# Kernel tuning notes

Measured on AMD Instinct MI355X. Metric: run time of the kernel, lower is better.

Reference implementation:

```python
import jax, jax.numpy as jnp
import numpy as np

N, E, D, L, G = 50000, 800000, 96, 4, 256
FI, PI, EI = 128, 16, 16


def setup_inputs() -> dict:
    key = jax.random.key(0)
    ks = jax.random.split(key, 40)
    w = lambda k, s: (jax.random.normal(k, s, jnp.float32) * 0.02)
    inp = {
        'h': jax.random.normal(ks[0], (N, FI), jnp.float32),
        'e': jax.random.normal(ks[1], (E, EI), jnp.float32),
        'p': jax.random.normal(ks[2], (N, PI), jnp.float32),
        'edge_index': jax.random.randint(ks[3], (2, E), 0, N),
        'batch': jnp.sort(jax.random.randint(ks[4], (N,), 0, G)),
        # embedding linears
        'h_emb_w': w(ks[5], (FI, D)), 'h_emb_b': jnp.zeros((D,), jnp.float32),
        'e_emb_w': w(ks[6], (EI, D)), 'e_emb_b': jnp.zeros((D,), jnp.float32),
        'p_emb_w': w(ks[7], (PI, D)), 'p_emb_b': jnp.zeros((D,), jnp.float32),
        # per-layer weights, stacked over L layers
        'gate_w': w(ks[8], (L, 3 * D, D)), 'gate_b': jnp.zeros((L, D), jnp.float32),
        'hps_w': w(ks[9], (L, 2 * D, D)), 'hps_b': jnp.zeros((L, D), jnp.float32),
        'hpr_w': w(ks[10], (L, 2 * D, D)), 'hpr_b': jnp.zeros((L, D), jnp.float32),
        'ps_w': w(ks[11], (L, D, D)), 'ps_b': jnp.zeros((L, D), jnp.float32),
        'pr_w': w(ks[12], (L, D, D)), 'pr_b': jnp.zeros((L, D), jnp.float32),
        # readout MLP
        'ro1_w': w(ks[13], (2 * D, D)), 'ro1_b': jnp.zeros((D,), jnp.float32),
        'ro2_w': w(ks[14], (D, 1)), 'ro2_b': jnp.zeros((1,), jnp.float32),
    }
    return inp


def reference(h, e, p, edge_index, batch,
              h_emb_w, h_emb_b, e_emb_w, e_emb_b, p_emb_w, p_emb_b,
              gate_w, gate_b, hps_w, hps_b, hpr_w, hpr_b,
              ps_w, ps_b, pr_w, pr_b, ro1_w, ro1_b, ro2_w, ro2_b):
    send, rec = edge_index[0], edge_index[1]
    n_nodes = h.shape[0]
    h = h @ h_emb_w + h_emb_b
    e = e @ e_emb_w + e_emb_b
    p = p @ p_emb_w + p_emb_b
    n_layers = gate_w.shape[0]
    for l in range(n_layers):
        # gather h at send/rec, gate over concat [E, 3D]
        eta_hat = jax.nn.sigmoid(
            jnp.concatenate([h[send], h[rec], e], axis=1) @ gate_w[l] + gate_b[l])
        eta = eta_hat / jnp.sum(eta_hat, axis=1, keepdims=True)
        hp = jnp.concatenate([h, p], axis=1)  # [N, 2D]
        h_msg = eta * (hp[send] @ hps_w[l] + hps_b[l])
        h_agg = jax.ops.segment_sum(h_msg, rec, num_segments=n_nodes)
        h_new = hp @ hpr_w[l] + hpr_b[l] + h_agg
        p_msg = eta * (p[send] @ ps_w[l] + ps_b[l])
        p_agg = jax.ops.segment_sum(p_msg, rec, num_segments=n_nodes)
        p_new = h_new @ pr_w[l] + pr_b[l] + p_agg  # uses updated h (matches torch layer)
        h = h + jax.nn.relu(h_new)
        e = e + jax.nn.relu(eta_hat)
        p = p + jnp.tanh(p_new)
    h_pool = jax.ops.segment_sum(h, batch, num_segments=G)  # global_add_pool
    p_pool = jax.ops.segment_sum(p, batch, num_segments=G)
    x = jnp.concatenate([h_pool, p_pool], axis=1) @ ro1_w + ro1_b
    x = jax.nn.relu(x) @ ro2_w + ro2_b
    return x.squeeze(-1)  # [G]
```

## Files before the change

### kernel.cpp

```cpp
#include <hip/hip_runtime.h>

typedef unsigned short u16;
typedef unsigned int u32;

#define NN 50000
#define EE 800000
#define DD 96
#define LL 4
#define GG 256
#define NPW 8
#define NPB (4*NPW)

typedef __bf16 bf16x8 __attribute__((ext_vector_type(8)));
typedef float f32x4 __attribute__((ext_vector_type(4)));

__device__ __forceinline__ u16 f2bf(float x){
  u32 u = __float_as_uint(x);
  u32 r = (u + 0x7FFFu + ((u >> 16) & 1u)) >> 16;
  return (u16)r;
}
__device__ __forceinline__ float bf2f(u16 b){
  return __uint_as_float(((u32)b) << 16);
}
__device__ __forceinline__ float bfx(const uint4& q, int i){
  u32 w = (i < 2) ? q.x : (i < 4) ? q.y : (i < 6) ? q.z : q.w;
  u32 h = (i & 1) ? (w >> 16) : (w & 0xFFFFu);
  return __uint_as_float(h << 16);
}
union BQ { uint4 q; bf16x8 v; };
__device__ __forceinline__ bf16x8 asbf(uint4 q){ BQ u; u.q = q; return u.v; }
__device__ __forceinline__ f32x4 mfma16(uint4 a, uint4 b, f32x4 c){
  return __builtin_amdgcn_mfma_f32_16x16x32_bf16(asbf(a), asbf(b), c, 0, 0, 0);
}
__device__ __forceinline__ uint4 pack8(const float* v){
  uint4 q;
  q.x = (u32)f2bf(v[0]) | ((u32)f2bf(v[1]) << 16);
  q.y = (u32)f2bf(v[2]) | ((u32)f2bf(v[3]) << 16);
  q.z = (u32)f2bf(v[4]) | ((u32)f2bf(v[5]) << 16);
  q.w = (u32)f2bf(v[6]) | ((u32)f2bf(v[7]) << 16);
  return q;
}
__device__ __forceinline__ uint4 packrow(const float* hsrc, const float* psrc, int row, int kbase){
  const float* src = (kbase < 96) ? (hsrc + (size_t)row*96 + kbase)
                                  : (psrc + (size_t)row*96 + (kbase - 96));
  float4 a0 = ((const float4*)src)[0];
  float4 a1 = ((const float4*)src)[1];
  float v[8] = {a0.x,a0.y,a0.z,a0.w,a1.x,a1.y,a1.z,a1.w};
  return pack8(v);
}

__global__ void k_diag(float* out, float val){
  int i = blockIdx.x*64 + threadIdx.x;
  if (i < GG) out[i] = val;
}

__global__ void k_zero(int* counts){
  int i = blockIdx.x*256 + threadIdx.x;
  if (i < NN) counts[i] = 0;
}
__global__ void k_hist(const int* rec, int* counts){
  int e = blockIdx.x*256 + threadIdx.x;
  if (e < EE) atomicAdd(&counts[rec[e]], 1);
}
__global__ void k_scan(const int* counts, int* cursor, int* node_start){
  __shared__ int wsum[16];
  __shared__ int carry_s;
  const int tid = threadIdx.x, lane = tid & 63, wid = tid >> 6;
  if (tid == 0) carry_s = 0;
  __syncthreads();
  for (int base = 0; base < NN; base += 1024){
    int i = base + tid;
    int v = (i < NN) ? counts[i] : 0;
    int x = v;
    #pragma unroll
    for (int d = 1; d < 64; d <<= 1){
      int t = __shfl_up(x, d);
      if (lane >= d) x += t;
    }
    if (lane == 63) wsum[wid] = x;
    __syncthreads();
    if (wid == 0 && lane < 16){
      int y = wsum[lane];
      #pragma unroll
      for (int d = 1; d < 16; d <<= 1){ int t = __shfl_up(y, d); if (lane >= d) y += t; }
      wsum[lane] = y;
    }
    __syncthreads();
    int woff = (wid == 0) ? 0 : wsum[wid-1];
    if (i < NN){
      int ex = carry_s + woff + x - v;
      cursor[i] = ex;
      node_start[i] = ex;
    }
    __syncthreads();
    if (tid == 1023) carry_s += wsum[15];
    __syncthreads();
  }
  if (tid == 0) node_start[NN] = EE;
}
__global__ void k_scatter(const int* send, const int* rec, int* cursor,
                          int* ss, int* rs, int* perm){
  int e = blockIdx.x*256 + threadIdx.x;
  if (e >= EE) return;
  int r = rec[e];
  int pos = atomicAdd(&cursor[r], 1);
  ss[pos] = send[e];
  rs[pos] = r;
  perm[pos] = e;
}

__global__ void k_prep(const float* gate_w, const float* gate_b,
    const float* hps_w, const float* hps_b,
    const float* hpr_w, const float* hpr_b,
    const float* ps_w, const float* ps_b,
    const float* pr_w,
    const float* h_emb_w, const float* p_emb_w, const float* e_emb_w,
    u16* Wt_cat, float* bias_cat, u16* Wt_e, u16* Wt_pr, u16* Wt_emb, u16* Wt_ee){
  int i = blockIdx.x*256 + threadIdx.x;
  const int S0 = LL*480*192, S1 = LL*96*96, S2 = LL*96*96, S3 = 192*160, S4 = 96*32, S5 = LL*480;
  if (i < S0){
    int l = i / (480*192); int r = i % (480*192);
    int j = r / 192, k = r % 192;
    int g = j / 96, jj = j % 96;
    float v = 0.f;
    if (g == 0){ if (k < 96) v = gate_w[((size_t)l*288 + k)*96 + jj]; }
    else if (g == 1){ if (k < 96) v = gate_w[((size_t)l*288 + 96 + k)*96 + jj]; }
    else if (g == 2){ if (k >= 96) v = ps_w[((size_t)l*96 + (k-96))*96 + jj]; }
    else if (g == 3){ v = hps_w[((size_t)l*192 + k)*96 + jj]; }
    else            { v = hpr_w[((size_t)l*192 + k)*96 + jj]; }
    Wt_cat[i] = f2bf(v);
    return;
  }
  i -= S0;
  if (i < S1){
    int l = i / 9216, r = i % 9216; int j = r / 96, k = r % 96;
    Wt_e[i] = f2bf(gate_w[((size_t)l*288 + 192 + k)*96 + j]);
    return;
  }
  i -= S1;
  if (i < S2){
    int l = i / 9216, r = i % 9216; int j = r / 96, k = r % 96;
    Wt_pr[i] = f2bf(pr_w[((size_t)l*96 + k)*96 + j]);
    return;
  }
  i -= S2;
  if (i < S3){
    int j = i / 160, k = i % 160;
    float v = 0.f;
    if (j < 96){ if (k < 128) v = h_emb_w[k*96 + j]; }
    else { if (k >= 128 && k < 144) v = p_emb_w[(k-128)*96 + (j-96)]; }
    Wt_emb[i] = f2bf(v);
    return;
  }
  i -= S3;
  if (i < S4){
    int j = i / 32, k = i % 32;
    Wt_ee[i] = f2bf(k < 16 ? e_emb_w[k*96 + j] : 0.f);
    return;
  }
  i -= S4;
  if (i < S5){
    int l = i / 480, j = i % 480;
    int g = j / 96, jj = j % 96;
    float v = 0.f;
    if (g == 1) v = gate_b[l*96 + jj];
    else if (g == 2) v = ps_b[l*96 + jj];
    else if (g == 3) v = hps_b[l*96 + jj];
    else if (g == 4) v = hpr_b[l*96 + jj];
    bias_cat[i] = v;
  }
}

__global__ __launch_bounds__(256,2) void k_emb_hp(const float* h_in, const float* p_in,
    const u16* Wt_emb, const float* h_emb_b, const float* p_emb_b,
    float* h, float* p){
  __shared__ u16 lds[96*168];
  const int tid = threadIdx.x;
  const int j0 = blockIdx.y * 96;
  for (int c = tid; c < 96*160/8; c += 256){
    int jr = c / 20, kc = c % 20;
    *(uint4*)&lds[jr*168 + kc*8] = *(const uint4*)(Wt_emb + (size_t)(j0+jr)*160 + kc*8);
  }
  __syncthreads();
  const int wave = tid >> 6, lane = tid & 63;
  const int quad = lane >> 4, l15 = lane & 15;
  const int base = blockIdx.x*256 + wave*64;
  f32x4 zero = {0.f,0.f,0.f,0.f};
  f32x4 acc[4][6];
  #pragma unroll
  for (int rg=0; rg<4; ++rg){
    #pragma unroll
    for (int ct=0; ct<6; ++ct) acc[rg][ct] = zero;
  }
  for (int ks = 0; ks < 5; ++ks){
    uint4 aq[4];
    #pragma unroll
    for (int rg = 0; rg < 4; ++rg){
      int row = base + rg*16 + l15;
      int chunk = ks*4 + quad;
      float v[8] = {0.f,0.f,0.f,0.f,0.f,0.f,0.f,0.f};
      if (row < NN){
        if (chunk < 16){
          const float4* sp = (const float4*)(h_in + (size_t)row*128 + chunk*8);
          float4 a0 = sp[0], a1 = sp[1];
          v[0]=a0.x; v[1]=a0.y; v[2]=a0.z; v[3]=a0.w; v[4]=a1.x; v[5]=a1.y; v[6]=a1.z; v[7]=a1.w;
        } else if (chunk < 18){
          const float4* sp = (const float4*)(p_in + (size_t)row*16 + (chunk-16)*8);
          float4 a0 = sp[0], a1 = sp[1];
          v[0]=a0.x; v[1]=a0.y; v[2]=a0.z; v[3]=a0.w; v[4]=a1.x; v[5]=a1.y; v[6]=a1.z; v[7]=a1.w;
        }
      }
      aq[rg] = pack8(v);
    }
    #pragma unroll
    for (int ct = 0; ct < 6; ++ct){
      uint4 bq = *(const uint4*)&lds[(ct*16+l15)*168 + ks*32 + quad*8];
      #pragma unroll
      for (int rg = 0; rg < 4; ++rg) acc[rg][ct] = mfma16(aq[rg], bq, acc[rg][ct]);
    }
  }
  #pragma unroll
  for (int rg=0; rg<4; ++rg){
    #pragma unroll
    for (int ct=0; ct<6; ++ct){
      #pragma unroll
      for (int reg=0; reg<4; ++reg){
        int row = base + rg*16 + quad*4 + reg;
        if (row < NN){
          int col = j0 + ct*16 + l15;
          float v = acc[rg][ct][reg] + (col < 96 ? h_emb_b[col] : p_emb_b[col-96]);
          if (col < 96) h[(size_t)row*96 + col] = v;
          else          p[(size_t)row*96 + col - 96] = v;
        }
      }
    }
  }
}

__global__ __launch_bounds__(256,2) void k_emb_e(const float* e_in, const int* perm,
    const u16* Wt_ee, const float* e_emb_b, u16* e_bf){
  __shared__ u16 lds[96*40];
  const int tid = threadIdx.x;
  for (int c = tid; c < 96*32/8; c += 256){
    int jr = c >> 2, kc = c & 3;
    *(uint4*)&lds[jr*40 + kc*8] = *(const uint4*)(Wt_ee + jr*32 + kc*8);
  }
  __syncthreads();
  const int wave = tid >> 6, lane = tid & 63;
  const int quad = lane >> 4, l15 = lane & 15;
  const int base = blockIdx.x*256 + wave*64;
  f32x4 zero = {0.f,0.f,0.f,0.f};
  f32x4 acc[4][6];
  #pragma unroll
  for (int rg=0; rg<4; ++rg){
    #pragma unroll
    for (int ct=0; ct<6; ++ct) acc[rg][ct] = zero;
  }
  uint4 aq[4];
  #pragma unroll
  for (int rg = 0; rg < 4; ++rg){
    int row = base + rg*16 + l15;
    int src = perm[row];
    float v[8] = {0.f,0.f,0.f,0.f,0.f,0.f,0.f,0.f};
    if (quad < 2){
      const float4* sp = (const float4*)(e_in + (size_t)src*16 + quad*8);
      float4 a0 = sp[0], a1 = sp[1];
      v[0]=a0.x; v[1]=a0.y; v[2]=a0.z; v[3]=a0.w; v[4]=a1.x; v[5]=a1.y; v[6]=a1.z; v[7]=a1.w;
    }
    aq[rg] = pack8(v);
  }
  #pragma unroll
  for (int ct = 0; ct < 6; ++ct){
    uint4 bq = *(const uint4*)&lds[(ct*16+l15)*40 + quad*8];
    #pragma unroll
    for (int rg = 0; rg < 4; ++rg) acc[rg][ct] = mfma16(aq[rg], bq, acc[rg][ct]);
  }
  #pragma unroll
  for (int rg=0; rg<4; ++rg){
    #pragma unroll
    for (int ct=0; ct<6; ++ct){
      #pragma unroll
      for (int reg=0; reg<4; ++reg){
        int row = base + rg*16 + quad*4 + reg;
        int col = ct*16 + l15;
        e_bf[(size_t)row*96 + col] = f2bf(acc[rg][ct][reg] + e_emb_b[col]);
      }
    }
  }
}

__global__ __launch_bounds__(256,2) void k_pre(const float* h, const float* p,
    const u16* Wt_cat, const float* bias_cat, int l,
    u16* Gt, float* h_agg){
  __shared__ u16 lds[96*200];
  const int tid = threadIdx.x;
  const int group = blockIdx.y;
  const u16* W = Wt_cat + ((size_t)l*480 + group*96)*192;
  for (int c = tid; c < 96*192/8; c += 256){
    int jr = c / 24, kc = c % 24;
    *(uint4*)&lds[jr*200 + kc*8] = *(const uint4*)(W + jr*192 + kc*8);
  }
  __syncthreads();
  const int wave = tid >> 6, lane = tid & 63;
  const int quad = lane >> 4, l15 = lane & 15;
  const int base = blockIdx.x*64 + wave*16;
  f32x4 zero = {0.f,0.f,0.f,0.f};
  f32x4 acc[6];
  #pragma unroll
  for (int ct=0; ct<6; ++ct) acc[ct] = zero;
  const int ks0 = (group == 2) ? 3 : 0;
  const int ks1 = (group <= 1) ? 3 : 6;
  uint4 zeroq = {0u,0u,0u,0u};
  const int arow = base + l15;
  for (int ks = ks0; ks < ks1; ++ks){
    int kbase = ks*32 + quad*8;
    uint4 aq = (arow < NN) ? packrow(h, p, arow, kbase) : zeroq;
    #pragma unroll
    for (int ct = 0; ct < 6; ++ct){
      uint4 bq = *(const uint4*)&lds[(ct*16+l15)*200 + ks*32 + quad*8];
      acc[ct] = mfma16(aq, bq, acc[ct]);
    }
  }
  const float* bptr = bias_cat + l*480 + group*96;
  if (group == 4){
    #pragma unroll
    for (int ct=0; ct<6; ++ct){
      #pragma unroll
      for (int reg=0; reg<4; ++reg){
        int row = base + quad*4 + reg;
        if (row < NN){
          int col = ct*16 + l15;
          h_agg[(size_t)row*96 + col] = acc[ct][reg] + bptr[col];
        }
      }
    }
  } else {
    float bv[6];
    #pragma unroll
    for (int ct=0; ct<6; ++ct) bv[ct] = bptr[ct*16 + l15];
    #pragma unroll
    for (int reg=0; reg<4; ++reg){
      int row = base + quad*4 + reg;
      if (row < NN){
        float v[8];
        #pragma unroll
        for (int ct=0; ct<6; ++ct) v[ct] = acc[ct][reg] + bv[ct];
        v[6] = 0.f; v[7] = 0.f;
        *(uint4*)(Gt + (size_t)row*512 + group*128 + l15*8) = pack8(v);
      }
    }
  }
}

__global__ __launch_bounds__(256,3) void k_edge(u16* e_bf, const u16* Wt_e_l,
    const int* ss, const int* rs, const int* node_start,
    const u16* Gt, float* h_agg, float* p_agg){
  __shared__ u16 lds[96*104];
  __shared__ float accLDS[4][2][NPW*96];
  const int tid = threadIdx.x;
  for (int c = tid; c < 96*96/8; c += 256){
    int jr = c / 12, kc = c % 12;
    *(uint4*)&lds[jr*104 + kc*8] = *(const uint4*)(Wt_e_l + jr*96 + kc*8);
  }
  __syncthreads();
  const int wave = tid >> 6, lane = tid & 63;
  const int quad = lane >> 4, l15 = lane & 15;
  const int n0 = blockIdx.x*NPB + wave*NPW;
  if (n0 >= NN) return;
  const int n1 = min(n0 + NPW, NN);
  const int ws0 = node_start[n0], ws1 = node_start[n1];
  float* accH = accLDS[wave][0];
  float* accP = accLDS[wave][1];
  for (int k = lane; k < NPW*96; k += 64){ accH[k] = 0.f; accP[k] = 0.f; }

  for (int tb = ws0; tb < ws1; tb += 64){
    f32x4 zero = {0.f,0.f,0.f,0.f};
    f32x4 acc[4][6];
    #pragma unroll
    for (int rg=0; rg<4; ++rg){
      #pragma unroll
      for (int ct=0; ct<6; ++ct) acc[rg][ct] = zero;
    }
    #pragma unroll
    for (int ks = 0; ks < 3; ++ks){
      uint4 aq[4];
      #pragma unroll
      for (int rg = 0; rg < 4; ++rg){
        int row = tb + rg*16 + l15;
        if (row > EE-1) row = EE-1;
        aq[rg] = *(const uint4*)(e_bf + (size_t)row*96 + ks*32 + quad*8);
      }
      #pragma unroll
      for (int ct = 0; ct < 6; ++ct){
        uint4 bq = *(const uint4*)&lds[(ct*16+l15)*104 + ks*32 + quad*8];
        #pragma unroll
        for (int rg = 0; rg < 4; ++rg) acc[rg][ct] = mfma16(aq[rg], bq, acc[rg][ct]);
      }
    }
    #pragma unroll
    for (int rg=0; rg<4; ++rg){
      const int e0 = tb + rg*16 + quad*4;
      if (e0 >= ws1) continue;
      int4 s4 = *(const int4*)(ss + e0);
      int4 r4 = *(const int4*)(rs + e0);
      const int sArr[4] = {s4.x, s4.y, s4.z, s4.w};
      const int rArr[4] = {r4.x, r4.y, r4.z, r4.w};
      float hacc[6], pacc[6];
      #pragma unroll
      for (int ct=0; ct<6; ++ct){ hacc[ct]=0.f; pacc[ct]=0.f; }
      int curR = rArr[0];
      uint4 grq = *(const uint4*)(Gt + (size_t)curR*512 + 128 + l15*8);
      #pragma unroll
      for (int reg=0; reg<4; ++reg){
        const int edge = e0 + reg;
        if (edge < ws1){
          const int s = sArr[reg], r = rArr[reg];
          if (r != curR){
            int nb = (curR - n0)*96;
            #pragma unroll
            for (int ct=0; ct<6; ++ct){
              int col = ct*16 + l15;
              atomicAdd(&accH[nb+col], hacc[ct]);
              atomicAdd(&accP[nb+col], pacc[ct]);
              hacc[ct]=0.f; pacc[ct]=0.f;
            }
            curR = r;
            grq = *(const uint4*)(Gt + (size_t)curR*512 + 128 + l15*8);
          }
          const u16* Gs = Gt + (size_t)s*512 + l15*8;
          uint4 aqv = *(const uint4*)(Gs);
          uint4 sqv = *(const uint4*)(Gs + 256);
          uint4 mqv = *(const uint4*)(Gs + 384);
          float eh[6]; float rsum = 0.f;
          #pragma unroll
          for (int ct=0; ct<6; ++ct){
            float z = acc[rg][ct][reg] + bfx(aqv, ct) + bfx(grq, ct);
            float v = 1.f/(1.f + __expf(-z));
            eh[ct] = v; rsum += v;
          }
          rsum += __shfl_xor(rsum, 1); rsum += __shfl_xor(rsum, 2);
          rsum += __shfl_xor(rsum, 4); rsum += __shfl_xor(rsum, 8);
          float inv = 1.f / rsum;
          #pragma unroll
          for (int ct=0; ct<6; ++ct){
            int col = ct*16 + l15;
            size_t ei = (size_t)edge*96 + col;
            e_bf[ei] = f2bf(bf2f(e_bf[ei]) + eh[ct]);
            float eta = eh[ct] * inv;
            hacc[ct] += eta * bfx(mqv, ct);
            pacc[ct] += eta * bfx(sqv, ct);
          }
        }
      }
      {
        int nb = (curR - n0)*96;
        #pragma unroll
        for (int ct=0; ct<6; ++ct){
          int col = ct*16 + l15;
          atomicAdd(&accH[nb+col], hacc[ct]);
          atomicAdd(&accP[nb+col], pacc[ct]);
        }
      }
    }
  }
  const int nk = (n1 - n0)*96;
  for (int k = lane; k < nk; k += 64){
    size_t gi = (size_t)n0*96 + k;
    h_agg[gi] += accH[k];
    p_agg[gi]  = accP[k];
  }
}

__global__ __launch_bounds__(256,2) void k_pr(const float* h_agg, const u16* Wt_pr_l,
    const float* pr_b_l, const float* p_agg, float* p, float* h){
  __shared__ u16 lds[96*104];
  const int tid = threadIdx.x;
  for (int c = tid; c < 96*96/8; c += 256){
    int jr = c / 12, kc = c % 12;
    *(uint4*)&lds[jr*104 + kc*8] = *(const uint4*)(Wt_pr_l + jr*96 + kc*8);
  }
  __syncthreads();
  const int wave = tid >> 6, lane = tid & 63;
  const int quad = lane >> 4, l15 = lane & 15;
  const int base = blockIdx.x*64 + wave*16;
  f32x4 zero = {0.f,0.f,0.f,0.f};
  f32x4 acc[6];
  #pragma unroll
  for (int ct=0; ct<6; ++ct) acc[ct] = zero;
  uint4 zeroq = {0u,0u,0u,0u};
  const int arow = base + l15;
  #pragma unroll
  for (int ks = 0; ks < 3; ++ks){
    int kbase = ks*32 + quad*8;
    uint4 aq = (arow < NN) ? packrow(h_agg, h_agg, arow, kbase) : zeroq;
    #pragma unroll
    for (int ct = 0; ct < 6; ++ct){
      uint4 bq = *(const uint4*)&lds[(ct*16+l15)*104 + ks*32 + quad*8];
      acc[ct] = mfma16(aq, bq, acc[ct]);
    }
  }
  #pragma unroll
  for (int ct=0; ct<6; ++ct){
    #pragma unroll
    for (int reg=0; reg<4; ++reg){
      int row = base + quad*4 + reg;
      if (row < NN){
        int col = ct*16 + l15;
        size_t idx = (size_t)row*96 + col;
        float v = acc[ct][reg] + pr_b_l[col] + p_agg[idx];
        float vv = fminf(fmaxf(v, -15.f), 15.f);
        float ex = __expf(2.f*vv);
        float th = (ex - 1.f) / (ex + 1.f);
        p[idx] += th;
        h[idx] += fmaxf(h_agg[idx], 0.f);
      }
    }
  }
}

__global__ void k_off(const int* batch, int* starts){
  int g = threadIdx.x;
  int lo = 0, hi = NN;
  while (lo < hi){ int mid = (lo + hi) >> 1; if (batch[mid] < g) lo = mid + 1; else hi = mid; }
  starts[g] = lo;
  if (g == 0) starts[GG] = NN;
}

__global__ void k_pool(const float* h, const float* p, const int* starts, float* pool){
  int g = blockIdx.x, t = threadIdx.x;
  int a = starts[g], b = starts[g+1];
  const float* src = (t < 96) ? h : p;
  int c = (t < 96) ? t : (t - 96);
  float s = 0.f;
  for (int n = a; n < b; ++n) s += src[(size_t)n*96 + c];
  pool[g*192 + t] = s;
}

__global__ void k_ro(const float* pool, const float* ro1_w, const float* ro1_b,
                     const float* ro2_w, const float* ro2_b, float* out){
  __shared__ float red[96];
  int g = blockIdx.x, j = threadIdx.x;
  if (j < 96){
    float a = ro1_b[j];
    for (int k = 0; k < 192; ++k) a += pool[g*192 + k] * ro1_w[k*96 + j];
    red[j] = fmaxf(a, 0.f) * ro2_w[j];
  }
  __syncthreads();
  if (j == 0){
    float s = 0.f;
    for (int k = 0; k < 96; ++k) s += red[k];
    out[g] = s + ro2_b[0];
  }
}

extern "C" void kernel_launch(void* const* d_in, const int* in_sizes, int n_in,
                              void* d_out, int out_size, void* d_ws, size_t ws_size,
                              hipStream_t stream){
  const float* in_h    = (const float*)d_in[0];
  const float* in_e    = (const float*)d_in[1];
  const float* in_p    = (const float*)d_in[2];
  const int*   eidx    = (const int*)d_in[3];
  const int*   batch   = (const int*)d_in[4];
  const float* h_emb_w = (const float*)d_in[5];
  const float* h_emb_b = (const float*)d_in[6];
  const float* e_emb_w = (const float*)d_in[7];
  const float* e_emb_b = (const float*)d_in[8];
  const float* p_emb_w = (const float*)d_in[9];
  const float* p_emb_b = (const float*)d_in[10];
  const float* gate_w  = (const float*)d_in[11];
  const float* gate_b  = (const float*)d_in[12];
  const float* hps_w   = (const float*)d_in[13];
  const float* hps_b   = (const float*)d_in[14];
  const float* hpr_w   = (const float*)d_in[15];
  const float* hpr_b   = (const float*)d_in[16];
  const float* ps_w    = (const float*)d_in[17];
  const float* ps_b    = (const float*)d_in[18];
  const float* pr_w    = (const float*)d_in[19];
  const float* pr_b    = (const float*)d_in[20];
  const float* ro1_w   = (const float*)d_in[21];
  const float* ro1_b   = (const float*)d_in[22];
  const float* ro2_w   = (const float*)d_in[23];
  const float* ro2_b   = (const float*)d_in[24];
  float* out = (float*)d_out;
  (void)in_sizes; (void)n_in; (void)out_size;

  u16* Gt = (u16*)d_in[1];

  char* w = (char*)d_ws;
  size_t off = 0;
  auto alloc = [&](size_t bytes)->char*{
    char* pt = w + off;
    off = (off + bytes + 255) & ~(size_t)255;
    return pt;
  };
  u16*   e_bf     = (u16*)alloc((size_t)EE*96*2);
  float* h        = (float*)alloc((size_t)NN*96*4);
  float* p        = (float*)alloc((size_t)NN*96*4);
  float* h_agg    = (float*)alloc((size_t)NN*96*4);
  float* p_agg    = (float*)alloc((size_t)NN*96*4);
  u16*   Wt_cat   = (u16*)alloc((size_t)LL*480*192*2);
  u16*   Wt_e     = (u16*)alloc((size_t)LL*96*96*2);
  u16*   Wt_pr    = (u16*)alloc((size_t)LL*96*96*2);
  float* bias_cat = (float*)alloc((size_t)LL*480*4);
  int*   perm     = (int*)alloc((size_t)EE*4);
  int*   ss       = (int*)alloc((size_t)EE*4);
  int*   rs       = (int*)alloc((size_t)EE*4);
  int*   counts   = (int*)alloc((size_t)NN*4);
  int*   cursor   = (int*)alloc((size_t)NN*4);
  int*   node_start = (int*)alloc((size_t)(NN+1)*4);
  char*  scratch  = alloc(197888);
  u16*   Wt_emb   = (u16*)scratch;
  u16*   Wt_ee    = (u16*)(scratch + 61440);
  float* pool     = (float*)scratch;
  int*   starts   = (int*)(scratch + 196608);
  const size_t NEED = off;

  if (ws_size < NEED){
    k_diag<<<4, 64, 0, stream>>>(out, (float)(ws_size >> 20));
    return;
  }

  const int* send = eidx;
  const int* rec  = eidx + EE;

  k_zero<<<196, 256, 0, stream>>>(counts);
  k_hist<<<3125, 256, 0, stream>>>(rec, counts);
  k_scan<<<1, 1024, 0, stream>>>(counts, cursor, node_start);
  k_scatter<<<3125, 256, 0, stream>>>(send, rec, cursor, ss, rs, perm);

  k_prep<<<1868, 256, 0, stream>>>(gate_w, gate_b, hps_w, hps_b, hpr_w, hpr_b,
      ps_w, ps_b, pr_w, h_emb_w, p_emb_w, e_emb_w,
      Wt_cat, bias_cat, Wt_e, Wt_pr, Wt_emb, Wt_ee);
  k_emb_hp<<<dim3(196,2), 256, 0, stream>>>(in_h, in_p, Wt_emb, h_emb_b, p_emb_b, h, p);
  k_emb_e<<<3125, 256, 0, stream>>>(in_e, perm, Wt_ee, e_emb_b, e_bf);

  const int edge_blocks = (NN + NPB - 1) / NPB;
  const int row_blocks  = (NN + 63) / 64;
  for (int l = 0; l < LL; ++l){
    k_pre<<<dim3(row_blocks,5), 256, 0, stream>>>(h, p, Wt_cat, bias_cat, l, Gt, h_agg);
    k_edge<<<edge_blocks, 256, 0, stream>>>(e_bf, Wt_e + (size_t)l*96*96, ss, rs,
                                            node_start, Gt, h_agg, p_agg);
    k_pr<<<row_blocks, 256, 0, stream>>>(h_agg, Wt_pr + (size_t)l*96*96, pr_b + l*96,
                                         p_agg, p, h);
  }

  k_off<<<1, 256, 0, stream>>>(batch, starts);
  k_pool<<<GG, 192, 0, stream>>>(h, p, starts, pool);
  k_ro<<<GG, 128, 0, stream>>>(pool, ro1_w, ro1_b, ro2_w, ro2_b, out);
}
```

Before: 2.174 ms.

## Stage edge-state updates through LDS and skip last-layer edge writeback

The edge kernel now loads each edge tile's bf16 features into registers once and keeps them. Previously each edge did a scalar 2-byte read-modify-write of e per column. Instead the sigmoid outputs are staged in a per-wave LDS buffer, added to the register-held tile, and written back as coalesced 16-byte stores. The final layer skips the edge update entirely because e is never read afterwards. The cost is more registers and LDS, so occupancy drops from 3 to 2 blocks per SIMD.

```diff
diff --git a/kernel.cpp b/kernel.cpp
--- a/kernel.cpp
+++ b/kernel.cpp
@@ -26,6 +26,16 @@
   u32 w = (i < 2) ? q.x : (i < 4) ? q.y : (i < 6) ? q.z : q.w;
   u32 h = (i & 1) ? (w >> 16) : (w & 0xFFFFu);
   return __uint_as_float(h << 16);
+}
+__device__ __forceinline__ u32 bfadd2(u32 a, u32 b){
+  float a0 = __uint_as_float(a << 16), a1 = __uint_as_float(a & 0xFFFF0000u);
+  float b0 = __uint_as_float(b << 16), b1 = __uint_as_float(b & 0xFFFF0000u);
+  return (u32)f2bf(a0 + b0) | ((u32)f2bf(a1 + b1) << 16);
+}
+__device__ __forceinline__ uint4 bfadd8(uint4 a, uint4 b){
+  uint4 r; r.x = bfadd2(a.x,b.x); r.y = bfadd2(a.y,b.y);
+  r.z = bfadd2(a.z,b.z); r.w = bfadd2(a.w,b.w);
+  return r;
 }
 union BQ { uint4 q; bf16x8 v; };
 __device__ __forceinline__ bf16x8 asbf(uint4 q){ BQ u; u.q = q; return u.v; }
@@ -352,11 +362,12 @@
   }
 }
 
-__global__ __launch_bounds__(256,3) void k_edge(u16* e_bf, const u16* Wt_e_l,
+__global__ __launch_bounds__(256,2) void k_edge(u16* e_bf, const u16* Wt_e_l,
     const int* ss, const int* rs, const int* node_start,
-    const u16* Gt, float* h_agg, float* p_agg){
+    const u16* Gt, float* h_agg, float* p_agg, int storeE){
   __shared__ u16 lds[96*104];
   __shared__ float accLDS[4][2][NPW*96];
+  __shared__ u16 stageLDS[4][16*104];
   const int tid = threadIdx.x;
   for (int c = tid; c < 96*96/8; c += 256){
     int jr = c / 12, kc = c % 12;
@@ -371,9 +382,19 @@
   const int ws0 = node_start[n0], ws1 = node_start[n1];
   float* accH = accLDS[wave][0];
   float* accP = accLDS[wave][1];
+  u16* stage = stageLDS[wave];
   for (int k = lane; k < NPW*96; k += 64){ accH[k] = 0.f; accP[k] = 0.f; }
 
   for (int tb = ws0; tb < ws1; tb += 64){
+    uint4 aq[4][3];
+    #pragma unroll
+    for (int rg = 0; rg < 4; ++rg){
+      int row = tb + rg*16 + l15;
+      if (row > EE-1) row = EE-1;
+      const u16* ep = e_bf + (size_t)row*96 + quad*8;
+      #pragma unroll
+      for (int ks = 0; ks < 3; ++ks) aq[rg][ks] = *(const uint4*)(ep + ks*32);
+    }
     f32x4 zero = {0.f,0.f,0.f,0.f};
     f32x4 acc[4][6];
     #pragma unroll
@@ -383,82 +404,92 @@
     }
     #pragma unroll
     for (int ks = 0; ks < 3; ++ks){
-      uint4 aq[4];
-      #pragma unroll
-      for (int rg = 0; rg < 4; ++rg){
-        int row = tb + rg*16 + l15;
-        if (row > EE-1) row = EE-1;
-        aq[rg] = *(const uint4*)(e_bf + (size_t)row*96 + ks*32 + quad*8);
-      }
       #pragma unroll
       for (int ct = 0; ct < 6; ++ct){
         uint4 bq = *(const uint4*)&lds[(ct*16+l15)*104 + ks*32 + quad*8];
         #pragma unroll
-        for (int rg = 0; rg < 4; ++rg) acc[rg][ct] = mfma16(aq[rg], bq, acc[rg][ct]);
+        for (int rg = 0; rg < 4; ++rg) acc[rg][ct] = mfma16(aq[rg][ks], bq, acc[rg][ct]);
       }
     }
     #pragma unroll
     for (int rg=0; rg<4; ++rg){
-      const int e0 = tb + rg*16 + quad*4;
-      if (e0 >= ws1) continue;
-      int4 s4 = *(const int4*)(ss + e0);
-      int4 r4 = *(const int4*)(rs + e0);
-      const int sArr[4] = {s4.x, s4.y, s4.z, s4.w};
-      const int rArr[4] = {r4.x, r4.y, r4.z, r4.w};
-      float hacc[6], pacc[6];
-      #pragma unroll
-      for (int ct=0; ct<6; ++ct){ hacc[ct]=0.f; pacc[ct]=0.f; }
-      int curR = rArr[0];
-      uint4 grq = *(const uint4*)(Gt + (size_t)curR*512 + 128 + l15*8);
-      #pragma unroll
-      for (int reg=0; reg<4; ++reg){
-        const int edge = e0 + reg;
-        if (edge < ws1){
-          const int s = sArr[reg], r = rArr[reg];
-          if (r != curR){
-            int nb = (curR - n0)*96;
+      const int tbr = tb + rg*16;
+      if (tbr >= ws1) break;
+      const int e0 = tbr + quad*4;
+      if (e0 < ws1){
+        int4 s4 = *(const int4*)(ss + e0);
+        int4 r4 = *(const int4*)(rs + e0);
+        const int sArr[4] = {s4.x, s4.y, s4.z, s4.w};
+        const int rArr[4] = {r4.x, r4.y, r4.z, r4.w};
+        float hacc[6], pacc[6];
+        #pragma unroll
+        for (int ct=0; ct<6; ++ct){ hacc[ct]=0.f; pacc[ct]=0.f; }
+        int curR = rArr[0];
+        uint4 grq = *(const uint4*)(Gt + (size_t)curR*512 + 128 + l15*8);
+        #pragma unroll
+        for (int reg=0; reg<4; ++reg){
+          const int edge = e0 + reg;
+          if (edge < ws1){
+            const int s = sArr[reg], r = rArr[reg];
+            if (r != curR){
+              int nb = (curR - n0)*96;
+              #pragma unroll
+              for (int ct=0; ct<6; ++ct){
+                int col = ct*16 + l15;
+                atomicAdd(&accH[nb+col], hacc[ct]);
+                atomicAdd(&accP[nb+col], pacc[ct]);
+                hacc[ct]=0.f; pacc[ct]=0.f;
+              }
+              curR = r;
+              grq = *(const uint4*)(Gt + (size_t)curR*512 + 128 + l15*8);
+            }
+            const u16* Gs = Gt + (size_t)s*512 + l15*8;
+            uint4 aqv = *(const uint4*)(Gs);
+            uint4 sqv = *(const uint4*)(Gs + 256);
+            uint4 mqv = *(const uint4*)(Gs + 384);
+            float eh[6]; float rsum = 0.f;
             #pragma unroll
             for (int ct=0; ct<6; ++ct){
-              int col = ct*16 + l15;
-              atomicAdd(&accH[nb+col], hacc[ct]);
-              atomicAdd(&accP[nb+col], pacc[ct]);
-              hacc[ct]=0.f; pacc[ct]=0.f;
+              float z = acc[rg][ct][reg] + bfx(aqv, ct) + bfx(grq, ct);
+              float v = 1.f/(1.f + __expf(-z));
+              eh[ct] = v; rsum += v;
             }
-            curR = r;
-            grq = *(const uint4*)(Gt + (size_t)curR*512 + 128 + l15*8);
+            rsum += __shfl_xor(rsum, 1); rsum += __shfl_xor(rsum, 2);
+            rsum += __shfl_xor(rsum, 4); rsum += __shfl_xor(rsum, 8);
+            float inv = 1.f / rsum;
+            if (storeE){
+              const int rr = quad*4 + reg;
+              #pragma unroll
+              for (int ct=0; ct<6; ++ct)
+                stage[rr*104 + ct*16 + l15] = f2bf(eh[ct]);
+            }
+            #pragma unroll
+            for (int ct=0; ct<6; ++ct){
+              float eta = eh[ct] * inv;
+              hacc[ct] += eta * bfx(mqv, ct);
+              pacc[ct] += eta * bfx(sqv, ct);
+            }
           }
-          const u16* Gs = Gt + (size_t)s*512 + l15*8;
-          uint4 aqv = *(const uint4*)(Gs);
-          uint4 sqv = *(const uint4*)(Gs + 256);
-          uint4 mqv = *(const uint4*)(Gs + 384);
-          float eh[6]; float rsum = 0.f;
-          #pragma unroll
-          for (int ct=0; ct<6; ++ct){
-            float z = acc[rg][ct][reg] + bfx(aqv, ct) + bfx(grq, ct);
-            float v = 1.f/(1.f + __expf(-z));
-            eh[ct] = v; rsum += v;
-          }
-          rsum += __shfl_xor(rsum, 1); rsum += __shfl_xor(rsum, 2);
-          rsum += __shfl_xor(rsum, 4); rsum += __shfl_xor(rsum, 8);
-          float inv = 1.f / rsum;
+        }
+        {
+          int nb = (curR - n0)*96;
           #pragma unroll
           for (int ct=0; ct<6; ++ct){
             int col = ct*16 + l15;
-            size_t ei = (size_t)edge*96 + col;
-            e_bf[ei] = f2bf(bf2f(e_bf[ei]) + eh[ct]);
-            float eta = eh[ct] * inv;
-            hacc[ct] += eta * bfx(mqv, ct);
-            pacc[ct] += eta * bfx(sqv, ct);
+            atomicAdd(&accH[nb+col], hacc[ct]);
+            atomicAdd(&accP[nb+col], pacc[ct]);
           }
         }
       }
-      {
-        int nb = (curR - n0)*96;
-        #pragma unroll
-        for (int ct=0; ct<6; ++ct){
-          int col = ct*16 + l15;
-          atomicAdd(&accH[nb+col], hacc[ct]);
-          atomicAdd(&accP[nb+col], pacc[ct]);
+      if (storeE){
+        const int row = tbr + l15;
+        if (row < ws1){
+          u16* ep = e_bf + (size_t)row*96 + quad*8;
+          #pragma unroll
+          for (int ks=0; ks<3; ++ks){
+            uint4 ehq = *(const uint4*)&stage[l15*104 + ks*32 + quad*8];
+            *(uint4*)(ep + ks*32) = bfadd8(aq[rg][ks], ehq);
+          }
         }
       }
     }
@@ -639,7 +670,8 @@
   for (int l = 0; l < LL; ++l){
     k_pre<<<dim3(row_blocks,5), 256, 0, stream>>>(h, p, Wt_cat, bias_cat, l, Gt, h_agg);
     k_edge<<<edge_blocks, 256, 0, stream>>>(e_bf, Wt_e + (size_t)l*96*96, ss, rs,
-                                            node_start, Gt, h_agg, p_agg);
+                                            node_start, Gt, h_agg, p_agg,
+                                            (l < LL-1) ? 1 : 0);
     k_pr<<<row_blocks, 256, 0, stream>>>(h_agg, Wt_pr + (size_t)l*96*96, pr_b + l*96,
                                          p_agg, p, h);
   }
```

Measured after the change: 2.280 ms. 4.9% more time.
